# Kernel optimization log

Measured on AMD Instinct MI355X. Metric: run time of the kernel, lower is better.

## Reference

```python
import jax, jax.numpy as jnp
import numpy as np

L, B, D, H = 2048, 2, 1024, 16
DK = D // H
SCALE = DK ** -0.5


def setup_inputs() -> dict:
    key = jax.random.key(0)
    ks = jax.random.split(key, 11)
    w_std = D ** -0.5
    return {
        "query": jax.random.normal(ks[0], (L, B, D), dtype=jnp.float32),
        "key": jax.random.normal(ks[1], (L, B, D), dtype=jnp.float32),
        "value": jax.random.normal(ks[2], (L, B, D), dtype=jnp.float32),
        "WQ_w": jax.random.normal(ks[3], (D, D), dtype=jnp.float32) * w_std,
        "WQ_b": jnp.zeros((D,), dtype=jnp.float32),
        "WK_w": jax.random.normal(ks[4], (D, D), dtype=jnp.float32) * w_std,
        "WK_b": jnp.zeros((D,), dtype=jnp.float32),
        "WV_w": jax.random.normal(ks[5], (D, D), dtype=jnp.float32) * w_std,
        "WV_b": jnp.zeros((D,), dtype=jnp.float32),
        "WO_w": jax.random.normal(ks[6], (D, D), dtype=jnp.float32) * w_std,
        "WO_b": jnp.zeros((D,), dtype=jnp.float32),
    }


def reference(query, key, value, WQ_w, WQ_b, WK_w, WK_b, WV_w, WV_b, WO_w, WO_b):
    tgt_len, batch, _ = query.shape
    src_len = key.shape[0]
    # linear projections (torch Linear: x @ W^T + b)
    q = (query @ WQ_w.T + WQ_b) * SCALE            # [L, B, D]
    k = key @ WK_w.T + WK_b                        # [S, B, D]
    v = value @ WV_w.T + WV_b                      # [S, B, D]
    # split heads: [len, B, D] -> [B*H, len, DK]
    q = q.reshape(tgt_len, batch * H, DK).transpose(1, 0, 2)
    k = k.reshape(src_len, batch * H, DK).transpose(1, 0, 2)
    v = v.reshape(src_len, batch * H, DK).transpose(1, 0, 2)
    # attention scores and softmax (full [B*H, L, S] matrix, as in the original)
    scores = jnp.einsum('nld,nsd->nls', q, k)      # [B*H, L, S]
    probs = jax.nn.softmax(scores, axis=-1)
    out = jnp.einsum('nls,nsd->nld', probs, v)     # [B*H, L, DK]
    # merge heads: [B*H, L, DK] -> [L, B, D]
    out = out.transpose(1, 0, 2).reshape(tgt_len, batch, D)
    return out @ WO_w.T + WO_b
```

## Files before the change

### kernel.cpp

```cpp
#include <hip/hip_runtime.h>
#include <hip/hip_fp16.h>

#define LL 2048
#define BB 2
#define DD 1024
#define HH 16
#define DKK 64

typedef _Float16 h8 __attribute__((ext_vector_type(8)));
typedef _Float16 h4 __attribute__((ext_vector_type(4)));
typedef float f4 __attribute__((ext_vector_type(4)));
typedef float f16v __attribute__((ext_vector_type(16)));

#define BAR() do {                                              \
    asm volatile("s_waitcnt lgkmcnt(0)" ::: "memory");          \
    __builtin_amdgcn_s_barrier();                               \
    asm volatile("" ::: "memory");                              \
} while (0)

__device__ __forceinline__ void gload_lds16(const void* g, void* l) {
    __builtin_amdgcn_global_load_lds(
        (const __attribute__((address_space(1))) void*)g,
        (__attribute__((address_space(3))) void*)l, 16, 0, 0);
}

__global__ __launch_bounds__(256) void cvt_all(
    const float* __restrict__ x0, const float* __restrict__ x1,
    const float* __restrict__ x2, const float* __restrict__ w0,
    const float* __restrict__ w1, const float* __restrict__ w2,
    const float* __restrict__ w3,
    _Float16* __restrict__ y0, _Float16* __restrict__ y1,
    _Float16* __restrict__ y2, _Float16* __restrict__ z0,
    _Float16* __restrict__ z1, _Float16* __restrict__ z2,
    _Float16* __restrict__ z3)
{
    const int sel = blockIdx.y;
    if (sel >= 3 && blockIdx.x >= 512) return;
    const float* src = (sel == 0) ? x0 : (sel == 1) ? x1 : (sel == 2) ? x2
                     : (sel == 3) ? w0 : (sel == 4) ? w1 : (sel == 5) ? w2 : w3;
    _Float16* dst = (sel == 0) ? y0 : (sel == 1) ? y1 : (sel == 2) ? y2
                  : (sel == 3) ? z0 : (sel == 4) ? z1 : (sel == 5) ? z2 : z3;
    const int i = (blockIdx.x * 256 + threadIdx.x) * 8;
    f4 a = *(const f4*)(src + i);
    f4 b = *(const f4*)(src + i + 4);
    h8 o = {(_Float16)a.x, (_Float16)a.y, (_Float16)a.z, (_Float16)a.w,
            (_Float16)b.x, (_Float16)b.y, (_Float16)b.z, (_Float16)b.w};
    *(h8*)(dst + i) = o;
}

__global__ __launch_bounds__(256) void qkv_proj(
    const _Float16* __restrict__ xq, const _Float16* __restrict__ xk,
    const _Float16* __restrict__ xv,
    const _Float16* __restrict__ wq, const float* __restrict__ bq,
    const _Float16* __restrict__ wk, const float* __restrict__ bk,
    const _Float16* __restrict__ wv, const float* __restrict__ bv,
    _Float16* __restrict__ qh, _Float16* __restrict__ kh,
    _Float16* __restrict__ vth)
{
    const int mode = blockIdx.z;
    const _Float16* X    = (mode == 0) ? xq : (mode == 1) ? xk : xv;
    const _Float16* W    = (mode == 0) ? wq : (mode == 1) ? wk : wv;
    const float*    bias = (mode == 0) ? bq : (mode == 1) ? bk : bv;

    __shared__ alignas(16) _Float16 a_sm[128 * 32];
    __shared__ alignas(16) _Float16 b_sm[128 * 32];

    const int tid  = threadIdx.x;
    const int lane = tid & 63;
    const int wave = tid >> 6;
    const int wm = (wave & 1) * 64;
    const int wn = (wave >> 1) * 64;
    const int m0 = blockIdx.x * 128;
    const int n0 = blockIdx.y * 128;

    const int srow = tid >> 2;
    const int scol = (tid & 3) * 8;
    const int lds_base = wave * 512;

    f4 acc[4][4];
    #pragma unroll
    for (int i = 0; i < 4; i++)
        #pragma unroll
        for (int j = 0; j < 4; j++)
            #pragma unroll
            for (int r = 0; r < 4; r++) acc[i][j][r] = 0.f;

    const int fr = lane & 15;
    const int fk = (lane >> 4) * 8;

    for (int k0 = 0; k0 < DD; k0 += 32) {
        gload_lds16(X + (size_t)(m0 + srow) * DD + k0 + scol,       &a_sm[lds_base]);
        gload_lds16(X + (size_t)(m0 + 64 + srow) * DD + k0 + scol,  &a_sm[2048 + lds_base]);
        gload_lds16(W + (size_t)(n0 + srow) * DD + k0 + scol,       &b_sm[lds_base]);
        gload_lds16(W + (size_t)(n0 + 64 + srow) * DD + k0 + scol,  &b_sm[2048 + lds_base]);
        __syncthreads();
        h8 af[4], bfr[4];
        #pragma unroll
        for (int i = 0; i < 4; i++) af[i]  = *(const h8*)&a_sm[(wm + i * 16 + fr) * 32 + fk];
        #pragma unroll
        for (int j = 0; j < 4; j++) bfr[j] = *(const h8*)&b_sm[(wn + j * 16 + fr) * 32 + fk];
        #pragma unroll
        for (int i = 0; i < 4; i++)
            #pragma unroll
            for (int j = 0; j < 4; j++)
                acc[i][j] = __builtin_amdgcn_mfma_f32_16x16x32_f16(af[i], bfr[j], acc[i][j], 0, 0, 0);
        __syncthreads();
    }

    const int colc = lane & 15;
    const int rowb = (lane >> 4) * 4;
    #pragma unroll
    for (int i = 0; i < 4; i++) {
        #pragma unroll
        for (int j = 0; j < 4; j++) {
            const int nn = n0 + wn + j * 16 + colc;
            const float bval = bias[nn];
            #pragma unroll
            for (int reg = 0; reg < 4; reg++) {
                const int mm = m0 + wm + i * 16 + rowb + reg;
                float v = acc[i][j][reg] + bval;
                const int b = mm & 1, l = mm >> 1;
                const int h = nn >> 6, dk = nn & 63;
                const int head = b * HH + h;
                if (mode == 0) {
                    v *= 0.1803368801111243f;
                    qh[((size_t)head * LL + l) * DKK + dk] = (_Float16)v;
                } else if (mode == 1) {
                    kh[((size_t)head * LL + l) * DKK + dk] = (_Float16)v;
                } else {
                    vth[((size_t)head * DKK + dk) * LL + l] = (_Float16)v;
                }
            }
        }
    }
}

__global__ __launch_bounds__(256, 2) void attn(
    const _Float16* __restrict__ qh, const _Float16* __restrict__ kh,
    const _Float16* __restrict__ vth, _Float16* __restrict__ oh)
{
    const int head = blockIdx.y;
    const int q0   = blockIdx.x * 128;
    const int tid = threadIdx.x, lane = tid & 63, wave = tid >> 6;
    const int qw = q0 + wave * 32;

    __shared__ alignas(16) _Float16 k_sm[128][72];
    __shared__ alignas(16) _Float16 vt_sm[64][136];
    __shared__ alignas(16) _Float16 p_sm[4][32][136];

    const int rq = lane & 31;
    const int kb = (lane >> 5) * 8;
    const int tid8 = tid * 8;

    const _Float16* khead  = kh  + (size_t)head * LL * DKK;
    const _Float16* vthead = vth + (size_t)head * DKK * LL;

    const _Float16* qbase = qh + ((size_t)head * LL + qw + rq) * DKK;
    h8 qa[4];
    #pragma unroll
    for (int kf = 0; kf < 4; kf++) qa[kf] = *(const h8*)(qbase + kf * 16 + kb);

    f16v o0, o1;
    float lsum[16];
    #pragma unroll
    for (int r = 0; r < 16; r++) { o0[r] = 0.f; o1[r] = 0.f; lsum[r] = 0.f; }

    #pragma unroll
    for (int t = 0; t < 4; t++) {
        const int flat = t * 2048 + tid8;
        *(h8*)&k_sm[flat >> 6][flat & 63] = *(const h8*)(khead + flat);
        *(h8*)&vt_sm[flat >> 7][flat & 127] =
            *(const h8*)(vthead + (size_t)(flat >> 7) * LL + (flat & 127));
    }
    BAR();

    _Float16* pw = &p_sm[wave][0][0];
    const int prow = 4 * (lane >> 5);

    for (int it = 0; it < 16; ++it) {
        const int s1 = it * 128 + 128;
        const bool more = (s1 < LL);

        h8 kpre[4], vpre[4];
        if (more) {
            const _Float16* kg = khead + (size_t)s1 * DKK;
            #pragma unroll
            for (int t = 0; t < 4; t++) kpre[t] = *(const h8*)(kg + t * 2048 + tid8);
            #pragma unroll
            for (int t = 0; t < 4; t++) {
                const int flat = t * 2048 + tid8;
                vpre[t] = *(const h8*)(vthead + (size_t)(flat >> 7) * LL + s1 + (flat & 127));
            }
        }

        f16v sc[4];
        #pragma unroll
        for (int st = 0; st < 4; st++) {
            #pragma unroll
            for (int r = 0; r < 16; r++) sc[st][r] = 0.f;
            #pragma unroll
            for (int kf = 0; kf < 4; kf++) {
                h8 kf8 = *(const h8*)&k_sm[st * 32 + rq][kf * 16 + kb];
                sc[st] = __builtin_amdgcn_mfma_f32_32x32x16_f16(qa[kf], kf8, sc[st], 0, 0, 0);
            }
        }

        #pragma unroll
        for (int st = 0; st < 4; st++) {
            #pragma unroll
            for (int r = 0; r < 16; r++) {
                float p = __builtin_amdgcn_exp2f(sc[st][r]);
                lsum[r] += p;
                const int row = (r & 3) + 8 * (r >> 2) + prow;
                pw[row * 136 + st * 32 + rq] = (_Float16)p;
            }
        }
        asm volatile("s_waitcnt lgkmcnt(0)" ::: "memory");

        #pragma unroll
        for (int kf2 = 0; kf2 < 8; kf2++) {
            h8 pa = *(const h8*)&pw[rq * 136 + kf2 * 16 + kb];
            h8 b0 = *(const h8*)&vt_sm[rq][kf2 * 16 + kb];
            h8 b1 = *(const h8*)&vt_sm[32 + rq][kf2 * 16 + kb];
            o0 = __builtin_amdgcn_mfma_f32_32x32x16_f16(pa, b0, o0, 0, 0, 0);
            o1 = __builtin_amdgcn_mfma_f32_32x32x16_f16(pa, b1, o1, 0, 0, 0);
        }

        BAR();
        if (more) {
            #pragma unroll
            for (int t = 0; t < 4; t++) {
                const int flat = t * 2048 + tid8;
                *(h8*)&k_sm[flat >> 6][flat & 63] = kpre[t];
            }
            #pragma unroll
            for (int t = 0; t < 4; t++) {
                const int flat = t * 2048 + tid8;
                *(h8*)&vt_sm[flat >> 7][flat & 127] = vpre[t];
            }
            BAR();
        }
    }

    #pragma unroll
    for (int m = 1; m < 32; m <<= 1)
        #pragma unroll
        for (int r = 0; r < 16; r++) lsum[r] += __shfl_xor(lsum[r], m, 64);

    const int b = head >> 4, h = head & 15;
    #pragma unroll
    for (int r = 0; r < 16; r++) {
        const int row = (r & 3) + 8 * (r >> 2) + prow;
        const int ql = qw + row;
        const float inv = 1.0f / lsum[r];
        const size_t base = (size_t)(ql * BB + b) * DD + h * DKK;
        oh[base + rq]      = (_Float16)(o0[r] * inv);
        oh[base + 32 + rq] = (_Float16)(o1[r] * inv);
    }
}

__global__ __launch_bounds__(256) void out_proj(
    const _Float16* __restrict__ oh, const _Float16* __restrict__ wo,
    const float* __restrict__ bo, float* __restrict__ out)
{
    __shared__ alignas(16) _Float16 a_sm[64 * 32];
    __shared__ alignas(16) _Float16 b_sm[128 * 32];
    const int tid = threadIdx.x, lane = tid & 63, wave = tid >> 6;
    const int wm = (wave & 1) * 32, wn = (wave >> 1) * 64;
    const int m0 = blockIdx.x * 64, n0 = blockIdx.y * 128;

    const int srow = tid >> 2;
    const int scol = (tid & 3) * 8;
    const int lds_base = wave * 512;

    f4 acc[2][4];
    #pragma unroll
    for (int i = 0; i < 2; i++)
        #pragma unroll
        for (int j = 0; j < 4; j++)
            #pragma unroll
            for (int r = 0; r < 4; r++) acc[i][j][r] = 0.f;

    const int fr = lane & 15;
    const int fk = (lane >> 4) * 8;

    for (int k0 = 0; k0 < DD; k0 += 32) {
        gload_lds16(oh + (size_t)(m0 + srow) * DD + k0 + scol,      &a_sm[lds_base]);
        gload_lds16(wo + (size_t)(n0 + srow) * DD + k0 + scol,      &b_sm[lds_base]);
        gload_lds16(wo + (size_t)(n0 + 64 + srow) * DD + k0 + scol, &b_sm[2048 + lds_base]);
        __syncthreads();
        h8 af[2], bfr[4];
        #pragma unroll
        for (int i = 0; i < 2; i++) af[i]  = *(const h8*)&a_sm[(wm + i * 16 + fr) * 32 + fk];
        #pragma unroll
        for (int j = 0; j < 4; j++) bfr[j] = *(const h8*)&b_sm[(wn + j * 16 + fr) * 32 + fk];
        #pragma unroll
        for (int i = 0; i < 2; i++)
            #pragma unroll
            for (int j = 0; j < 4; j++)
                acc[i][j] = __builtin_amdgcn_mfma_f32_16x16x32_f16(af[i], bfr[j], acc[i][j], 0, 0, 0);
        __syncthreads();
    }

    const int colc = lane & 15;
    const int rowb = (lane >> 4) * 4;
    #pragma unroll
    for (int i = 0; i < 2; i++) {
        #pragma unroll
        for (int j = 0; j < 4; j++) {
            const int nn = n0 + wn + j * 16 + colc;
            const float bval = bo[nn];
            #pragma unroll
            for (int reg = 0; reg < 4; reg++) {
                const int mm = m0 + wm + i * 16 + rowb + reg;
                out[(size_t)mm * DD + nn] = acc[i][j][reg] + bval;
            }
        }
    }
}

extern "C" void kernel_launch(void* const* d_in, const int* in_sizes, int n_in,
                              void* d_out, int out_size, void* d_ws, size_t ws_size,
                              hipStream_t stream) {
    const float* qin = (const float*)d_in[0];
    const float* kin = (const float*)d_in[1];
    const float* vin = (const float*)d_in[2];
    const float* wq  = (const float*)d_in[3];
    const float* bq  = (const float*)d_in[4];
    const float* wk  = (const float*)d_in[5];
    const float* bk  = (const float*)d_in[6];
    const float* wv  = (const float*)d_in[7];
    const float* bv  = (const float*)d_in[8];
    const float* wo  = (const float*)d_in[9];
    const float* bo  = (const float*)d_in[10];

    const size_t seg = (size_t)32 * LL * DKK;
    _Float16* qh  = (_Float16*)d_ws;
    _Float16* kh  = qh + seg;
    _Float16* vth = kh + seg;
    _Float16* oh  = vth + seg;
    _Float16* wqh = oh + seg;
    _Float16* wkh = wqh + (size_t)DD * DD;
    _Float16* wvh = wkh + (size_t)DD * DD;
    _Float16* woh = wvh + (size_t)DD * DD;
    _Float16* xqh = woh + (size_t)DD * DD;
    _Float16* xkh = xqh + seg;
    _Float16* xvh = xkh + seg;

    hipLaunchKernelGGL(cvt_all, dim3(2048, 7), dim3(256), 0, stream,
                       qin, kin, vin, wq, wk, wv, wo,
                       xqh, xkh, xvh, wqh, wkh, wvh, woh);
    hipLaunchKernelGGL(qkv_proj, dim3(32, 8, 3), dim3(256), 0, stream,
                       xqh, xkh, xvh, wqh, bq, wkh, bk, wvh, bv, qh, kh, vth);
    hipLaunchKernelGGL(attn, dim3(16, 32), dim3(256), 0, stream, qh, kh, vth, oh);
    hipLaunchKernelGGL(out_proj, dim3(64, 8), dim3(256), 0, stream, oh, woh,
                       bo, (float*)d_out);
}
```

Before: 229.9 us.

## Keep attention probabilities in registers via transposed QK^T and lane shuffles

Swaps the MFMA operand order so the score tile comes out transposed, which lets each lane hold probabilities for a single query row. The P operand for the PV MFMA is then built in registers from packed fp16 pairs exchanged with __shfl_xor across the two half-waves, so the per-wave LDS round trip for P and its waitcnt are gone. The row sum collapses to one scalar per lane, with a single shuffle and a small LDS table for the final normalisation. The cost is extra shuffle and select instructions in the inner loop, plus some added risk in getting the lane-to-row mapping right.

```diff
diff --git a/kernel.cpp b/kernel.cpp
--- a/kernel.cpp
+++ b/kernel.cpp
@@ -22,6 +22,12 @@
     __builtin_amdgcn_global_load_lds(
         (const __attribute__((address_space(1))) void*)g,
         (__attribute__((address_space(3))) void*)l, 16, 0, 0);
+}
+
+__device__ __forceinline__ unsigned pack2h(float a, float b) {
+    union { _Float16 h[2]; unsigned u; } x;
+    x.h[0] = (_Float16)a; x.h[1] = (_Float16)b;
+    return x.u;
 }
 
 __global__ __launch_bounds__(256) void cvt_all(
@@ -146,10 +152,11 @@
 
     __shared__ alignas(16) _Float16 k_sm[128][72];
     __shared__ alignas(16) _Float16 vt_sm[64][136];
-    __shared__ alignas(16) _Float16 p_sm[4][32][136];
+    __shared__ float ls_sm[4][32];
 
     const int rq = lane & 31;
-    const int kb = (lane >> 5) * 8;
+    const int hi = lane >> 5;
+    const int kb = hi * 8;
     const int tid8 = tid * 8;
 
     const _Float16* khead  = kh  + (size_t)head * LL * DKK;
@@ -161,9 +168,9 @@
     for (int kf = 0; kf < 4; kf++) qa[kf] = *(const h8*)(qbase + kf * 16 + kb);
 
     f16v o0, o1;
-    float lsum[16];
-    #pragma unroll
-    for (int r = 0; r < 16; r++) { o0[r] = 0.f; o1[r] = 0.f; lsum[r] = 0.f; }
+    #pragma unroll
+    for (int r = 0; r < 16; r++) { o0[r] = 0.f; o1[r] = 0.f; }
+    float lsum = 0.f;
 
     #pragma unroll
     for (int t = 0; t < 4; t++) {
@@ -174,9 +181,6 @@
     }
     BAR();
 
-    _Float16* pw = &p_sm[wave][0][0];
-    const int prow = 4 * (lane >> 5);
-
     for (int it = 0; it < 16; ++it) {
         const int s1 = it * 128 + 128;
         const bool more = (s1 < LL);
@@ -201,29 +205,38 @@
             #pragma unroll
             for (int kf = 0; kf < 4; kf++) {
                 h8 kf8 = *(const h8*)&k_sm[st * 32 + rq][kf * 16 + kb];
-                sc[st] = __builtin_amdgcn_mfma_f32_32x32x16_f16(qa[kf], kf8, sc[st], 0, 0, 0);
+                sc[st] = __builtin_amdgcn_mfma_f32_32x32x16_f16(kf8, qa[kf], sc[st], 0, 0, 0);
             }
         }
 
         #pragma unroll
         for (int st = 0; st < 4; st++) {
+            float p[16];
             #pragma unroll
             for (int r = 0; r < 16; r++) {
-                float p = __builtin_amdgcn_exp2f(sc[st][r]);
-                lsum[r] += p;
-                const int row = (r & 3) + 8 * (r >> 2) + prow;
-                pw[row * 136 + st * 32 + rq] = (_Float16)p;
-            }
-        }
-        asm volatile("s_waitcnt lgkmcnt(0)" ::: "memory");
-
-        #pragma unroll
-        for (int kf2 = 0; kf2 < 8; kf2++) {
-            h8 pa = *(const h8*)&pw[rq * 136 + kf2 * 16 + kb];
-            h8 b0 = *(const h8*)&vt_sm[rq][kf2 * 16 + kb];
-            h8 b1 = *(const h8*)&vt_sm[32 + rq][kf2 * 16 + kb];
-            o0 = __builtin_amdgcn_mfma_f32_32x32x16_f16(pa, b0, o0, 0, 0, 0);
-            o1 = __builtin_amdgcn_mfma_f32_32x32x16_f16(pa, b1, o1, 0, 0, 0);
+                p[r] = __builtin_amdgcn_exp2f(sc[st][r]);
+                lsum += p[r];
+            }
+            unsigned own[4][2], part[4][2];
+            #pragma unroll
+            for (int g = 0; g < 4; g++) {
+                own[g][0] = pack2h(p[4 * g],     p[4 * g + 1]);
+                own[g][1] = pack2h(p[4 * g + 2], p[4 * g + 3]);
+                part[g][0] = __shfl_xor(own[g][0], 32, 64);
+                part[g][1] = __shfl_xor(own[g][1], 32, 64);
+            }
+            #pragma unroll
+            for (int j = 0; j < 2; j++) {
+                union { unsigned u[4]; h8 h; } pa;
+                pa.u[0] = hi ? part[2 * j + 1][0] : own[2 * j][0];
+                pa.u[1] = hi ? part[2 * j + 1][1] : own[2 * j][1];
+                pa.u[2] = hi ? own[2 * j + 1][0]  : part[2 * j][0];
+                pa.u[3] = hi ? own[2 * j + 1][1]  : part[2 * j][1];
+                h8 b0 = *(const h8*)&vt_sm[rq][st * 32 + j * 16 + kb];
+                h8 b1 = *(const h8*)&vt_sm[32 + rq][st * 32 + j * 16 + kb];
+                o0 = __builtin_amdgcn_mfma_f32_32x32x16_f16(pa.h, b0, o0, 0, 0, 0);
+                o1 = __builtin_amdgcn_mfma_f32_32x32x16_f16(pa.h, b1, o1, 0, 0, 0);
+            }
         }
 
         BAR();
@@ -242,17 +255,16 @@
         }
     }
 
-    #pragma unroll
-    for (int m = 1; m < 32; m <<= 1)
-        #pragma unroll
-        for (int r = 0; r < 16; r++) lsum[r] += __shfl_xor(lsum[r], m, 64);
+    lsum += __shfl_xor(lsum, 32, 64);
+    ls_sm[wave][rq] = 1.0f / lsum;
+    asm volatile("s_waitcnt lgkmcnt(0)" ::: "memory");
 
     const int b = head >> 4, h = head & 15;
     #pragma unroll
     for (int r = 0; r < 16; r++) {
-        const int row = (r & 3) + 8 * (r >> 2) + prow;
-        const int ql = qw + row;
-        const float inv = 1.0f / lsum[r];
+        const int qrow = (r & 3) + 8 * (r >> 2) + 4 * hi;
+        const float inv = ls_sm[wave][qrow];
+        const int ql = qw + qrow;
         const size_t base = (size_t)(ql * BB + b) * DD + h * DKK;
         oh[base + rq]      = (_Float16)(o0[r] * inv);
         oh[base + 32 + rq] = (_Float16)(o1[r] * inv);
```

Measured after the change: 229.1 us. Within noise of the previous version (-0.4%).
